# Kernel optimization log

Hardware: AMD Instinct MI355X
Metric: run time of the kernel (lower is better)

Reference implementation:

```python
import jax, jax.numpy as jnp
import numpy as np

B, L, D, NLAYERS, KCONV = 8, 2048, 1024, 3, 4


def setup_inputs() -> dict:
    key = jax.random.key(0)
    ks = jax.random.split(key, 8)
    inp = {
        "x": jax.random.normal(ks[0], (B, L, D), jnp.float32),
        "conv_w": jax.random.normal(ks[1], (NLAYERS, D, KCONV), jnp.float32) * 0.02,
        "conv_b": jnp.zeros((NLAYERS, D), jnp.float32),
        "wr_w": jax.random.normal(ks[2], (NLAYERS, D, D), jnp.float32) * (1.0 / np.sqrt(D)),
        "wr_b": jnp.zeros((NLAYERS, D), jnp.float32),
        "wi_w": jax.random.normal(ks[3], (NLAYERS, D, D), jnp.float32) * (1.0 / np.sqrt(D)),
        "wi_b": jnp.zeros((NLAYERS, D), jnp.float32),
        "log_a": 3.0 + 0.1 * jax.random.normal(ks[4], (NLAYERS, D), jnp.float32),
        "wo_w": jax.random.normal(ks[5], (NLAYERS, D, D), jnp.float32) * (1.0 / np.sqrt(D)),
        "norm_w": jnp.ones((NLAYERS, D), jnp.float32),
        "norm_out_w": jnp.ones((D,), jnp.float32),
    }
    return inp


def _rmsnorm(x, w, eps=1e-6):
    return x * w * jax.lax.rsqrt(jnp.mean(x * x, axis=-1, keepdims=True) + eps)


def _parallel_scan(a, b):
    # h_t = a_t * h_{t-1} + b_t  via log-space prefix scan (h0 = 0)
    a32 = a.astype(jnp.float32)
    b32 = b.astype(jnp.float32)
    log_A = jnp.cumsum(jnp.log(jnp.maximum(a32, 1e-7)), axis=1)
    log_A = jnp.maximum(log_A, -80.0)  # a<=1 so log_A<=0 already
    A = jnp.exp(log_A)
    h = A * jnp.cumsum(b32 * jnp.exp(-log_A), axis=1)
    return h.astype(a.dtype)


def _rglru_layer(x, cw, cb, wrw, wrb, wiw, wib, la, wow, nw):
    # causal depthwise conv1d, kernel 4, left pad 3
    Lx = x.shape[1]
    xp = jnp.pad(x, ((0, 0), (KCONV - 1, 0), (0, 0)))
    x_conv = cb + sum(xp[:, k:k + Lx, :] * cw[:, k] for k in range(KCONV))
    r_t = jax.nn.sigmoid(x_conv @ wrw.T + wrb)
    i_t = jax.nn.sigmoid(x_conv @ wiw.T + wib)
    a_base = jax.nn.sigmoid(la.astype(jnp.float32)).astype(x.dtype)
    a_t = a_base ** (8.0 * r_t)
    b_t = jnp.sqrt(jnp.clip(1.0 - a_t * a_t, 1e-6, None)) * (i_t * x_conv)
    h = _parallel_scan(a_t, b_t)
    return _rmsnorm(h @ wow.T, nw)


def reference(x, conv_w, conv_b, wr_w, wr_b, wi_w, wi_b, log_a, wo_w, norm_w, norm_out_w):
    h = x
    for l in range(NLAYERS):
        h = _rglru_layer(h, conv_w[l], conv_b[l], wr_w[l], wr_b[l],
                         wi_w[l], wi_b[l], log_a[l], wo_w[l], norm_w[l])
    return _rmsnorm(h, norm_out_w)
```

## Files before the change

### kernel.cpp

```cpp
#include <hip/hip_runtime.h>
#include <type_traits>

#define BDIM 8
#define LDIM 2048
#define DDIM 1024
#define NL 3
#define K4 4
#define MDIM (BDIM * LDIM)
#define BK32 32
#define NT32 (DDIM / BK32)

typedef __bf16 bf16x8 __attribute__((ext_vector_type(8)));
typedef __bf16 bf16x4 __attribute__((ext_vector_type(4)));
typedef float f32x4 __attribute__((ext_vector_type(4)));
typedef const __attribute__((address_space(1))) void gvoid_t;
typedef __attribute__((address_space(3))) void svoid_t;

__device__ __forceinline__ void load16(const void* g, void* lds_uniform) {
    __builtin_amdgcn_global_load_lds((gvoid_t*)g, (svoid_t*)lds_uniform, 16, 0, 0);
}

#define SBAR()                                  \
    do {                                        \
        asm volatile("" ::: "memory");          \
        __builtin_amdgcn_s_barrier();           \
        asm volatile("" ::: "memory");          \
    } while (0)
#define WAITV(N) asm volatile("s_waitcnt vmcnt(" #N ")" ::: "memory")
#define LGKM0() asm volatile("s_waitcnt lgkmcnt(0)" ::: "memory")

__global__ void cvt_bf16(const float* __restrict__ s, __bf16* __restrict__ d, int n) {
    int i = blockIdx.x * 256 + threadIdx.x;
    if (i < n) d[i] = (__bf16)s[i];
}

__global__ __launch_bounds__(256) void cvt_interleave(const float* __restrict__ wr,
                                                      const float* __restrict__ wi,
                                                      __bf16* __restrict__ w2, int n) {
    int i = blockIdx.x * 256 + threadIdx.x;
    if (i >= n) return;
    int k = i & (DDIM - 1);
    int ld = i >> 10;
    int l = ld >> 10;
    int d = ld & (DDIM - 1);
    size_t base = ((size_t)l * 2 * DDIM + 2 * d) * DDIM + k;
    w2[base] = (__bf16)wr[i];
    w2[base + DDIM] = (__bf16)wi[i];
}

template <typename T>
__global__ __launch_bounds__(256) void conv_kernel(const T* __restrict__ X,
                                                   const float* __restrict__ cw,
                                                   const float* __restrict__ cb,
                                                   __bf16* __restrict__ XC) {
    int idx = blockIdx.x * 256 + threadIdx.x;
    int d = (idx & (DDIM / 4 - 1)) << 2;
    int t = (idx >> 8) & (LDIM - 1);
    int b = idx >> 19;
    float wv[4][4];
    *(float4*)wv[0] = ((const float4*)cw)[d + 0];
    *(float4*)wv[1] = ((const float4*)cw)[d + 1];
    *(float4*)wv[2] = ((const float4*)cw)[d + 2];
    *(float4*)wv[3] = ((const float4*)cw)[d + 3];
    float4 cbv = *(const float4*)(cb + d);
    float acc[4] = {cbv.x, cbv.y, cbv.z, cbv.w};
#pragma unroll
    for (int k = 0; k < K4; k++) {
        int tt = t + k - (K4 - 1);
        if (tt >= 0) {
            size_t off = ((size_t)(b * LDIM + tt) << 10) + d;
            float xv[4];
            if constexpr (std::is_same<T, float>::value) {
                float4 v = *(const float4*)(X + off);
                xv[0] = v.x; xv[1] = v.y; xv[2] = v.z; xv[3] = v.w;
            } else {
                bf16x4 v = *(const bf16x4*)(X + off);
                xv[0] = (float)v.x; xv[1] = (float)v.y; xv[2] = (float)v.z; xv[3] = (float)v.w;
            }
#pragma unroll
            for (int j = 0; j < 4; j++) acc[j] += xv[j] * wv[j][k];
        }
    }
    bf16x4 o;
    o.x = (__bf16)acc[0]; o.y = (__bf16)acc[1]; o.z = (__bf16)acc[2]; o.w = (__bf16)acc[3];
    *(bf16x4*)(XC + ((size_t)(b * LDIM + t) << 10) + d) = o;
}

__global__ __launch_bounds__(512, 2) void gate_gemm(
    const __bf16* __restrict__ A, const __bf16* __restrict__ W2,
    const float* __restrict__ wrb, const float* __restrict__ wib,
    const float* __restrict__ la,
    __bf16* __restrict__ LOGA, __bf16* __restrict__ BB) {
    __shared__ __attribute__((aligned(16))) __bf16 sm[65536];
    int tid = threadIdx.x;
    int wave = tid >> 6, lane = tid & 63;
    int wm = wave >> 2, wn = wave & 3;
    int fr = lane & 15, quad = lane >> 4;

    int nx = gridDim.x;
    int bid = blockIdx.y * nx + blockIdx.x;
    int cpx = (nx * gridDim.y) >> 3;
    int sw = (bid & 7) * cpx + (bid >> 3);
    int bm0 = (sw / nx) * 256;
    int bn0 = (sw % nx) * 256;

    const __bf16* Ag = A + (size_t)bm0 * DDIM;
    const __bf16* Bg = W2 + (size_t)bn0 * DDIM;

    f32x4 acc[8][4];
    f32x4 zero = {0.f, 0.f, 0.f, 0.f};
#pragma unroll
    for (int i = 0; i < 8; i++)
#pragma unroll
        for (int j = 0; j < 4; j++) acc[i][j] = zero;

    int offA[2][4], offB[4];
#pragma unroll
    for (int mh = 0; mh < 2; mh++)
#pragma unroll
        for (int mi = 0; mi < 4; mi++) {
            int row = wm * 128 + (mh * 4 + mi) * 16 + fr;
            offA[mh][mi] = row * 32 + ((quad ^ ((row >> 1) & 3)) << 3);
        }
#pragma unroll
    for (int ni = 0; ni < 4; ni++) {
        int row = wn * 64 + ni * 16 + fr;
        offB[ni] = 8192 + row * 32 + ((quad ^ ((row >> 1) & 3)) << 3);
    }
    int r0 = tid >> 2, g0 = (tid & 3) ^ ((r0 >> 1) & 3);
    int r1 = (512 + tid) >> 2, g1 = ((512 + tid) & 3) ^ ((r1 >> 1) & 3);
    const __bf16* gA0 = Ag + (size_t)r0 * DDIM + g0 * 8;
    const __bf16* gA1 = Ag + (size_t)r1 * DDIM + g1 * 8;
    const __bf16* gB0 = Bg + (size_t)r0 * DDIM + g0 * 8;
    const __bf16* gB1 = Bg + (size_t)r1 * DDIM + g1 * 8;
    int lb0 = wave * 512, lb1 = 4096 + wave * 512;

    auto STAGEH = [&](int buf, int t, int j) {
        int lo = buf * 16384;
        if (j == 0) {
            load16(gA0 + t * BK32, sm + lo + lb0);
            load16(gB0 + t * BK32, sm + lo + 8192 + lb0);
        } else {
            load16(gA1 + t * BK32, sm + lo + lb1);
            load16(gB1 + t * BK32, sm + lo + 8192 + lb1);
        }
    };
    auto STAGE = [&](int buf, int t) { STAGEH(buf, t, 0); STAGEH(buf, t, 1); };

    STAGE(0, 0);
    STAGE(1, 1);
    STAGE(2, 2);
    for (int t4 = 0; t4 < NT32; t4 += 4) {
#pragma unroll
        for (int tt = 0; tt < 4; tt++) {
            int t = t4 + tt;
            if (t + 2 < NT32) { WAITV(8); }
            else if (t + 1 < NT32) { WAITV(4); }
            else { WAITV(0); }
            SBAR();
            const __bf16* base = sm + tt * 16384;
            int sb = (tt + 3) & 3;
            bf16x8 bfm[4], af[4];
            if (t + 3 < NT32) STAGEH(sb, t + 3, 0);
#pragma unroll
            for (int ni = 0; ni < 4; ni++) bfm[ni] = *(const bf16x8*)(base + offB[ni]);
#pragma unroll
            for (int mi = 0; mi < 4; mi++) af[mi] = *(const bf16x8*)(base + offA[0][mi]);
            SBAR();
            LGKM0();
            __builtin_amdgcn_s_setprio(1);
#pragma unroll
            for (int ni = 0; ni < 4; ni++)
#pragma unroll
                for (int mi = 0; mi < 4; mi++)
                    acc[mi][ni] = __builtin_amdgcn_mfma_f32_16x16x32_bf16(
                        af[mi], bfm[ni], acc[mi][ni], 0, 0, 0);
            __builtin_amdgcn_s_setprio(0);
            SBAR();
            if (t + 3 < NT32) STAGEH(sb, t + 3, 1);
#pragma unroll
            for (int mi = 0; mi < 4; mi++) af[mi] = *(const bf16x8*)(base + offA[1][mi]);
            SBAR();
            LGKM0();
            __builtin_amdgcn_s_setprio(1);
#pragma unroll
            for (int ni = 0; ni < 4; ni++)
#pragma unroll
                for (int mi = 0; mi < 4; mi++)
                    acc[4 + mi][ni] = __builtin_amdgcn_mfma_f32_16x16x32_bf16(
                        af[mi], bfm[ni], acc[4 + mi][ni], 0, 0, 0);
            __builtin_amdgcn_s_setprio(0);
        }
    }

    float* Lt = (float*)&sm[0];
    int colg = (tid & 31) * 8;
    int d0 = (bn0 >> 1) + (colg >> 1);
    float rb[4], ibv[4], lnab[4];
    {
        float4 r4 = *(const float4*)(wrb + d0);
        float4 i4 = *(const float4*)(wib + d0);
        float4 l4 = *(const float4*)(la + d0);
        float lav[4] = {l4.x, l4.y, l4.z, l4.w};
        rb[0] = r4.x; rb[1] = r4.y; rb[2] = r4.z; rb[3] = r4.w;
        ibv[0] = i4.x; ibv[1] = i4.y; ibv[2] = i4.z; ibv[3] = i4.w;
#pragma unroll
        for (int j = 0; j < 4; j++) lnab[j] = __logf(1.f / (1.f + __expf(-lav[j])));
    }
#pragma unroll
    for (int mi = 0; mi < 8; mi++) {
        __syncthreads();
#pragma unroll
        for (int ni = 0; ni < 4; ni++) {
            int col = wn * 64 + ni * 16 + fr;
#pragma unroll
            for (int reg = 0; reg < 4; reg++)
                Lt[(wm * 16 + quad * 4 + reg) * 260 + col] = acc[mi][ni][reg];
        }
        __syncthreads();
#pragma unroll
        for (int hf = 0; hf < 2; hf++) {
            int r = (tid >> 5) + hf * 16;
            int m = bm0 + (r >> 4) * 128 + mi * 16 + (r & 15);
            float vv[8];
            *(f32x4*)&vv[0] = *(const f32x4*)&Lt[r * 260 + colg];
            *(f32x4*)&vv[4] = *(const f32x4*)&Lt[r * 260 + colg + 4];
            bf16x4 xcv = *(const bf16x4*)(A + (size_t)m * DDIM + d0);
            bf16x4 og, ob;
#pragma unroll
            for (int j = 0; j < 4; j++) {
                float rv = 1.f / (1.f + __expf(-(vv[2 * j] + rb[j])));
                float iv = 1.f / (1.f + __expf(-(vv[2 * j + 1] + ibv[j])));
                float lga = 8.f * rv * lnab[j];
                float a = __expf(lga);
                float bt = sqrtf(fmaxf(1.f - a * a, 1e-6f)) * (iv * (float)xcv[j]);
                og[j] = (__bf16)lga;
                ob[j] = (__bf16)bt;
            }
            *(bf16x4*)(LOGA + (size_t)m * DDIM + d0) = og;
            *(bf16x4*)(BB + (size_t)m * DDIM + d0) = ob;
        }
    }
}

__global__ __launch_bounds__(512, 2) void out_gemm(
    const __bf16* __restrict__ A, const __bf16* __restrict__ Wo, __bf16* __restrict__ HW) {
    __shared__ __attribute__((aligned(16))) __bf16 sm[65536];
    int tid = threadIdx.x;
    int wave = tid >> 6, lane = tid & 63;
    int wm = wave >> 2, wn = wave & 3;
    int fr = lane & 15, quad = lane >> 4;

    int nx = gridDim.x;
    int bid = blockIdx.y * nx + blockIdx.x;
    int cpx = (nx * gridDim.y) >> 3;
    int sw = (bid & 7) * cpx + (bid >> 3);
    int bm0 = (sw / nx) * 256;
    int bn0 = (sw % nx) * 256;

    const __bf16* Ag = A + (size_t)bm0 * DDIM;
    const __bf16* Bg = Wo + (size_t)bn0 * DDIM;

    f32x4 acc[8][4];
    f32x4 zero = {0.f, 0.f, 0.f, 0.f};
#pragma unroll
    for (int i = 0; i < 8; i++)
#pragma unroll
        for (int j = 0; j < 4; j++) acc[i][j] = zero;

    int offA[2][4], offB[4];
#pragma unroll
    for (int mh = 0; mh < 2; mh++)
#pragma unroll
        for (int mi = 0; mi < 4; mi++) {
            int row = wm * 128 + (mh * 4 + mi) * 16 + fr;
            offA[mh][mi] = row * 32 + ((quad ^ ((row >> 1) & 3)) << 3);
        }
#pragma unroll
    for (int ni = 0; ni < 4; ni++) {
        int row = wn * 64 + ni * 16 + fr;
        offB[ni] = 8192 + row * 32 + ((quad ^ ((row >> 1) & 3)) << 3);
    }
    int r0 = tid >> 2, g0 = (tid & 3) ^ ((r0 >> 1) & 3);
    int r1 = (512 + tid) >> 2, g1 = ((512 + tid) & 3) ^ ((r1 >> 1) & 3);
    const __bf16* gA0 = Ag + (size_t)r0 * DDIM + g0 * 8;
    const __bf16* gA1 = Ag + (size_t)r1 * DDIM + g1 * 8;
    const __bf16* gB0 = Bg + (size_t)r0 * DDIM + g0 * 8;
    const __bf16* gB1 = Bg + (size_t)r1 * DDIM + g1 * 8;
    int lb0 = wave * 512, lb1 = 4096 + wave * 512;

    auto STAGEH = [&](int buf, int t, int j) {
        int lo = buf * 16384;
        if (j == 0) {
            load16(gA0 + t * BK32, sm + lo + lb0);
            load16(gB0 + t * BK32, sm + lo + 8192 + lb0);
        } else {
            load16(gA1 + t * BK32, sm + lo + lb1);
            load16(gB1 + t * BK32, sm + lo + 8192 + lb1);
        }
    };
    auto STAGE = [&](int buf, int t) { STAGEH(buf, t, 0); STAGEH(buf, t, 1); };

    STAGE(0, 0);
    STAGE(1, 1);
    STAGE(2, 2);
    for (int t4 = 0; t4 < NT32; t4 += 4) {
#pragma unroll
        for (int tt = 0; tt < 4; tt++) {
            int t = t4 + tt;
            if (t + 2 < NT32) { WAITV(8); }
            else if (t + 1 < NT32) { WAITV(4); }
            else { WAITV(0); }
            SBAR();
            const __bf16* base = sm + tt * 16384;
            int sb = (tt + 3) & 3;
            bf16x8 bfm[4], af[4];
            if (t + 3 < NT32) STAGEH(sb, t + 3, 0);
#pragma unroll
            for (int ni = 0; ni < 4; ni++) bfm[ni] = *(const bf16x8*)(base + offB[ni]);
#pragma unroll
            for (int mi = 0; mi < 4; mi++) af[mi] = *(const bf16x8*)(base + offA[0][mi]);
            SBAR();
            LGKM0();
            __builtin_amdgcn_s_setprio(1);
#pragma unroll
            for (int ni = 0; ni < 4; ni++)
#pragma unroll
                for (int mi = 0; mi < 4; mi++)
                    acc[mi][ni] = __builtin_amdgcn_mfma_f32_16x16x32_bf16(
                        af[mi], bfm[ni], acc[mi][ni], 0, 0, 0);
            __builtin_amdgcn_s_setprio(0);
            SBAR();
            if (t + 3 < NT32) STAGEH(sb, t + 3, 1);
#pragma unroll
            for (int mi = 0; mi < 4; mi++) af[mi] = *(const bf16x8*)(base + offA[1][mi]);
            SBAR();
            LGKM0();
            __builtin_amdgcn_s_setprio(1);
#pragma unroll
            for (int ni = 0; ni < 4; ni++)
#pragma unroll
                for (int mi = 0; mi < 4; mi++)
                    acc[4 + mi][ni] = __builtin_amdgcn_mfma_f32_16x16x32_bf16(
                        af[mi], bfm[ni], acc[4 + mi][ni], 0, 0, 0);
            __builtin_amdgcn_s_setprio(0);
        }
    }

    float* Lt = (float*)&sm[0];
    int colg = (tid & 31) * 8;
    int n0 = bn0 + colg;
#pragma unroll
    for (int mi = 0; mi < 8; mi++) {
        __syncthreads();
#pragma unroll
        for (int ni = 0; ni < 4; ni++) {
            int col = wn * 64 + ni * 16 + fr;
#pragma unroll
            for (int reg = 0; reg < 4; reg++)
                Lt[(wm * 16 + quad * 4 + reg) * 260 + col] = acc[mi][ni][reg];
        }
        __syncthreads();
#pragma unroll
        for (int hf = 0; hf < 2; hf++) {
            int r = (tid >> 5) + hf * 16;
            int m = bm0 + (r >> 4) * 128 + mi * 16 + (r & 15);
            float vv[8];
            *(f32x4*)&vv[0] = *(const f32x4*)&Lt[r * 260 + colg];
            *(f32x4*)&vv[4] = *(const f32x4*)&Lt[r * 260 + colg + 4];
            bf16x8 o;
#pragma unroll
            for (int j = 0; j < 8; j++) o[j] = (__bf16)vv[j];
            *(bf16x8*)(HW + (size_t)m * DDIM + n0) = o;
        }
    }
}

#define SCH 32
#define SCT 64
__global__ __launch_bounds__(1024) void scan_kernel(const __bf16* __restrict__ LOGA,
                                                    const __bf16* __restrict__ BB,
                                                    __bf16* __restrict__ H) {
    int b = blockIdx.y;
    int dl = threadIdx.x & 31;
    int d = blockIdx.x * 32 + dl;
    int c = threadIdx.x >> 5;
    size_t base = ((size_t)b * LDIM + (size_t)c * SCT) * DDIM + d;
    const __bf16* pga = LOGA + base;
    const __bf16* pbb = BB + base;
    __bf16* pH = H + base;

    float S = 0.f;
#pragma unroll 8
    for (int t = 0; t < SCT; t++) S += (float)pga[(size_t)t * DDIM];
    __shared__ float sS[SCH][32];
    sS[c][dl] = S;
    __syncthreads();
    float L0 = 0.f;
    for (int cc = 0; cc < c; cc++) L0 += sS[cc][dl];

    float Lr = L0, lcp = fmaxf(L0, -80.f), hB = 0.f;
#pragma unroll 4
    for (int t = 0; t < SCT; t++) {
        float lga = (float)pga[(size_t)t * DDIM];
        Lr += lga;
        float lc = fmaxf(Lr, -80.f);
        hB = __expf(lc - lcp) * hB + (float)pbb[(size_t)t * DDIM];
        lcp = lc;
    }
    float Ac = __expf(fmaxf(Lr, -80.f) - fmaxf(L0, -80.f));
    __shared__ float sA[SCH][32], sB[SCH][32];
    sA[c][dl] = Ac;
    sB[c][dl] = hB;
    __syncthreads();
    float hin = 0.f;
    for (int cc = 0; cc < c; cc++) hin = sA[cc][dl] * hin + sB[cc][dl];

    Lr = L0;
    lcp = fmaxf(L0, -80.f);
    float h = hin;
#pragma unroll 4
    for (int t = 0; t < SCT; t++) {
        float lga = (float)pga[(size_t)t * DDIM];
        Lr += lga;
        float lc = fmaxf(Lr, -80.f);
        h = __expf(lc - lcp) * h + (float)pbb[(size_t)t * DDIM];
        lcp = lc;
        pH[(size_t)t * DDIM] = (__bf16)h;
    }
}

template <typename TI, typename TO>
__global__ __launch_bounds__(256) void rmsnorm_kernel(const TI* __restrict__ X,
                                                      const float* __restrict__ w,
                                                      TO* __restrict__ Y) {
    int row = blockIdx.x;
    int tid = threadIdx.x;
    size_t off = (size_t)row * DDIM + tid * 4;
    float v[4];
    if constexpr (std::is_same<TI, float>::value) {
        float4 t = *(const float4*)(X + off);
        v[0] = t.x; v[1] = t.y; v[2] = t.z; v[3] = t.w;
    } else {
        bf16x4 t = *(const bf16x4*)(X + off);
        v[0] = (float)t.x; v[1] = (float)t.y; v[2] = (float)t.z; v[3] = (float)t.w;
    }
    float s = v[0] * v[0] + v[1] * v[1] + v[2] * v[2] + v[3] * v[3];
#pragma unroll
    for (int o = 32; o > 0; o >>= 1) s += __shfl_down(s, o);
    __shared__ float sw[4];
    if ((tid & 63) == 0) sw[tid >> 6] = s;
    __syncthreads();
    float tot = sw[0] + sw[1] + sw[2] + sw[3];
    float scale = rsqrtf(tot * (1.f / (float)DDIM) + 1e-6f);
    float4 wv = ((const float4*)w)[tid];
    float o0 = v[0] * wv.x * scale, o1 = v[1] * wv.y * scale;
    float o2 = v[2] * wv.z * scale, o3 = v[3] * wv.w * scale;
    if constexpr (std::is_same<TO, float>::value) {
        float4 o = {o0, o1, o2, o3};
        *(float4*)(Y + off) = o;
    } else {
        bf16x4 o;
        o.x = (__bf16)o0; o.y = (__bf16)o1; o.z = (__bf16)o2; o.w = (__bf16)o3;
        *(bf16x4*)(Y + off) = o;
    }
}

extern "C" void kernel_launch(void* const* d_in, const int* in_sizes, int n_in,
                              void* d_out, int out_size, void* d_ws, size_t ws_size,
                              hipStream_t stream) {
    const float* x = (const float*)d_in[0];
    const float* conv_w = (const float*)d_in[1];
    const float* conv_b = (const float*)d_in[2];
    const float* wr_w = (const float*)d_in[3];
    const float* wr_b = (const float*)d_in[4];
    const float* wi_w = (const float*)d_in[5];
    const float* wi_b = (const float*)d_in[6];
    const float* log_a = (const float*)d_in[7];
    const float* wo_w = (const float*)d_in[8];
    const float* norm_w = (const float*)d_in[9];
    const float* norm_out_w = (const float*)d_in[10];

    const size_t W2SZ = (size_t)NL * 2 * DDIM * DDIM;
    const size_t WOSZ = (size_t)NL * DDIM * DDIM;
    const size_t MD = (size_t)MDIM * DDIM;
    __bf16* w2 = (__bf16*)d_ws;
    __bf16* wo16 = w2 + W2SZ;
    __bf16* XC = wo16 + WOSZ;
    __bf16* LGA = XC + MD;
    __bf16* BBf = LGA + MD;
    __bf16* Hb = BBf + MD;
    __bf16* HWb = Hb + MD;
    __bf16* PNb = HWb + MD;

    int nw = (int)WOSZ;
    cvt_interleave<<<(nw + 255) / 256, 256, 0, stream>>>(wr_w, wi_w, w2, nw);
    cvt_bf16<<<(nw + 255) / 256, 256, 0, stream>>>(wo_w, wo16, nw);

    for (int l = 0; l < NL; l++) {
        if (l == 0)
            conv_kernel<float><<<(MDIM * (DDIM / 4)) / 256, 256, 0, stream>>>(
                x, conv_w, conv_b, XC);
        else
            conv_kernel<__bf16><<<(MDIM * (DDIM / 4)) / 256, 256, 0, stream>>>(
                PNb, conv_w + (size_t)l * DDIM * K4, conv_b + (size_t)l * DDIM, XC);
        gate_gemm<<<dim3(2 * DDIM / 256, MDIM / 256), 512, 0, stream>>>(
            XC, w2 + (size_t)l * 2 * DDIM * DDIM,
            wr_b + (size_t)l * DDIM, wi_b + (size_t)l * DDIM, log_a + (size_t)l * DDIM,
            LGA, BBf);
        scan_kernel<<<dim3(DDIM / 32, BDIM), 1024, 0, stream>>>(LGA, BBf, Hb);
        out_gemm<<<dim3(DDIM / 256, MDIM / 256), 512, 0, stream>>>(
            Hb, wo16 + (size_t)l * DDIM * DDIM, HWb);
        rmsnorm_kernel<__bf16, __bf16><<<MDIM, 256, 0, stream>>>(
            HWb, norm_w + (size_t)l * DDIM, PNb);
    }
    rmsnorm_kernel<__bf16, float><<<MDIM, 256, 0, stream>>>(PNb, norm_out_w, (float*)d_out);
}
```

Measured before the change: 919.0 us.

## Cut per-tile barriers to one and issue LDS reads via inline asm

Both GEMM main loops now use a single workgroup barrier per K-tile instead of four. All four global-to-LDS prefetch loads for tile t+3 are issued together right after that barrier. LDS fragment reads go through inline ds_read_b128 with precomputed LDS byte addresses, and sched_barrier fences keep the compiler from reordering them around the MFMA blocks. This removes barrier stalls and the split-stage ping-pong in exchange for less forced wave interleaving. Correctness relies on the 4-buffer ring and the vmcnt waits to keep buffers from being overwritten while other waves still read them.

```diff
diff --git a/kernel.cpp b/kernel.cpp
--- a/kernel.cpp
+++ b/kernel.cpp
@@ -28,6 +28,16 @@
     } while (0)
 #define WAITV(N) asm volatile("s_waitcnt vmcnt(" #N ")" ::: "memory")
 #define LGKM0() asm volatile("s_waitcnt lgkmcnt(0)" ::: "memory")
+#define SCHED0() __builtin_amdgcn_sched_barrier(0)
+
+__device__ __forceinline__ unsigned lds_addr(const void* p) {
+    return (unsigned)(unsigned long long)(svoid_t*)(p);
+}
+__device__ __forceinline__ bf16x8 dsr16(unsigned a) {
+    f32x4 r;
+    asm volatile("ds_read_b128 %0, %1" : "=v"(r) : "v"(a));
+    return __builtin_bit_cast(bf16x8, r);
+}
 
 __global__ void cvt_bf16(const float* __restrict__ s, __bf16* __restrict__ d, int n) {
     int i = blockIdx.x * 256 + threadIdx.x;
@@ -114,18 +124,19 @@
 #pragma unroll
         for (int j = 0; j < 4; j++) acc[i][j] = zero;
 
-    int offA[2][4], offB[4];
+    unsigned smb = lds_addr(sm);
+    unsigned adA[2][4], adB[4];
 #pragma unroll
     for (int mh = 0; mh < 2; mh++)
 #pragma unroll
         for (int mi = 0; mi < 4; mi++) {
             int row = wm * 128 + (mh * 4 + mi) * 16 + fr;
-            offA[mh][mi] = row * 32 + ((quad ^ ((row >> 1) & 3)) << 3);
+            adA[mh][mi] = smb + 2u * (row * 32 + ((quad ^ ((row >> 1) & 3)) << 3));
         }
 #pragma unroll
     for (int ni = 0; ni < 4; ni++) {
         int row = wn * 64 + ni * 16 + fr;
-        offB[ni] = 8192 + row * 32 + ((quad ^ ((row >> 1) & 3)) << 3);
+        adB[ni] = smb + 2u * (8192 + row * 32 + ((quad ^ ((row >> 1) & 3)) << 3));
     }
     int r0 = tid >> 2, g0 = (tid & 3) ^ ((r0 >> 1) & 3);
     int r1 = (512 + tid) >> 2, g1 = ((512 + tid) & 3) ^ ((r1 >> 1) & 3);
@@ -135,17 +146,13 @@
     const __bf16* gB1 = Bg + (size_t)r1 * DDIM + g1 * 8;
     int lb0 = wave * 512, lb1 = 4096 + wave * 512;
 
-    auto STAGEH = [&](int buf, int t, int j) {
+    auto STAGE = [&](int buf, int t) {
         int lo = buf * 16384;
-        if (j == 0) {
-            load16(gA0 + t * BK32, sm + lo + lb0);
-            load16(gB0 + t * BK32, sm + lo + 8192 + lb0);
-        } else {
-            load16(gA1 + t * BK32, sm + lo + lb1);
-            load16(gB1 + t * BK32, sm + lo + 8192 + lb1);
-        }
+        load16(gA0 + t * BK32, sm + lo + lb0);
+        load16(gA1 + t * BK32, sm + lo + lb1);
+        load16(gB0 + t * BK32, sm + lo + 8192 + lb0);
+        load16(gB1 + t * BK32, sm + lo + 8192 + lb1);
     };
-    auto STAGE = [&](int buf, int t) { STAGEH(buf, t, 0); STAGEH(buf, t, 1); };
 
     STAGE(0, 0);
     STAGE(1, 1);
@@ -158,16 +165,15 @@
             else if (t + 1 < NT32) { WAITV(4); }
             else { WAITV(0); }
             SBAR();
-            const __bf16* base = sm + tt * 16384;
-            int sb = (tt + 3) & 3;
+            if (t + 3 < NT32) STAGE((tt + 3) & 3, t + 3);
+            unsigned tb = (unsigned)(tt * 32768);
             bf16x8 bfm[4], af[4];
-            if (t + 3 < NT32) STAGEH(sb, t + 3, 0);
-#pragma unroll
-            for (int ni = 0; ni < 4; ni++) bfm[ni] = *(const bf16x8*)(base + offB[ni]);
-#pragma unroll
-            for (int mi = 0; mi < 4; mi++) af[mi] = *(const bf16x8*)(base + offA[0][mi]);
-            SBAR();
+#pragma unroll
+            for (int ni = 0; ni < 4; ni++) bfm[ni] = dsr16(adB[ni] + tb);
+#pragma unroll
+            for (int mi = 0; mi < 4; mi++) af[mi] = dsr16(adA[0][mi] + tb);
             LGKM0();
+            SCHED0();
             __builtin_amdgcn_s_setprio(1);
 #pragma unroll
             for (int ni = 0; ni < 4; ni++)
@@ -176,12 +182,10 @@
                     acc[mi][ni] = __builtin_amdgcn_mfma_f32_16x16x32_bf16(
                         af[mi], bfm[ni], acc[mi][ni], 0, 0, 0);
             __builtin_amdgcn_s_setprio(0);
-            SBAR();
-            if (t + 3 < NT32) STAGEH(sb, t + 3, 1);
-#pragma unroll
-            for (int mi = 0; mi < 4; mi++) af[mi] = *(const bf16x8*)(base + offA[1][mi]);
-            SBAR();
+#pragma unroll
+            for (int mi = 0; mi < 4; mi++) af[mi] = dsr16(adA[1][mi] + tb);
             LGKM0();
+            SCHED0();
             __builtin_amdgcn_s_setprio(1);
 #pragma unroll
             for (int ni = 0; ni < 4; ni++)
@@ -268,18 +272,19 @@
 #pragma unroll
         for (int j = 0; j < 4; j++) acc[i][j] = zero;
 
-    int offA[2][4], offB[4];
+    unsigned smb = lds_addr(sm);
+    unsigned adA[2][4], adB[4];
 #pragma unroll
     for (int mh = 0; mh < 2; mh++)
 #pragma unroll
         for (int mi = 0; mi < 4; mi++) {
             int row = wm * 128 + (mh * 4 + mi) * 16 + fr;
-            offA[mh][mi] = row * 32 + ((quad ^ ((row >> 1) & 3)) << 3);
+            adA[mh][mi] = smb + 2u * (row * 32 + ((quad ^ ((row >> 1) & 3)) << 3));
         }
 #pragma unroll
     for (int ni = 0; ni < 4; ni++) {
         int row = wn * 64 + ni * 16 + fr;
-        offB[ni] = 8192 + row * 32 + ((quad ^ ((row >> 1) & 3)) << 3);
+        adB[ni] = smb + 2u * (8192 + row * 32 + ((quad ^ ((row >> 1) & 3)) << 3));
     }
     int r0 = tid >> 2, g0 = (tid & 3) ^ ((r0 >> 1) & 3);
     int r1 = (512 + tid) >> 2, g1 = ((512 + tid) & 3) ^ ((r1 >> 1) & 3);
@@ -289,17 +294,13 @@
     const __bf16* gB1 = Bg + (size_t)r1 * DDIM + g1 * 8;
     int lb0 = wave * 512, lb1 = 4096 + wave * 512;
 
-    auto STAGEH = [&](int buf, int t, int j) {
+    auto STAGE = [&](int buf, int t) {
         int lo = buf * 16384;
-        if (j == 0) {
-            load16(gA0 + t * BK32, sm + lo + lb0);
-            load16(gB0 + t * BK32, sm + lo + 8192 + lb0);
-        } else {
-            load16(gA1 + t * BK32, sm + lo + lb1);
-            load16(gB1 + t * BK32, sm + lo + 8192 + lb1);
-        }
+        load16(gA0 + t * BK32, sm + lo + lb0);
+        load16(gA1 + t * BK32, sm + lo + lb1);
+        load16(gB0 + t * BK32, sm + lo + 8192 + lb0);
+        load16(gB1 + t * BK32, sm + lo + 8192 + lb1);
     };
-    auto STAGE = [&](int buf, int t) { STAGEH(buf, t, 0); STAGEH(buf, t, 1); };
 
     STAGE(0, 0);
     STAGE(1, 1);
@@ -312,16 +313,15 @@
             else if (t + 1 < NT32) { WAITV(4); }
             else { WAITV(0); }
             SBAR();
-            const __bf16* base = sm + tt * 16384;
-            int sb = (tt + 3) & 3;
+            if (t + 3 < NT32) STAGE((tt + 3) & 3, t + 3);
+            unsigned tb = (unsigned)(tt * 32768);
             bf16x8 bfm[4], af[4];
-            if (t + 3 < NT32) STAGEH(sb, t + 3, 0);
-#pragma unroll
-            for (int ni = 0; ni < 4; ni++) bfm[ni] = *(const bf16x8*)(base + offB[ni]);
-#pragma unroll
-            for (int mi = 0; mi < 4; mi++) af[mi] = *(const bf16x8*)(base + offA[0][mi]);
-            SBAR();
+#pragma unroll
+            for (int ni = 0; ni < 4; ni++) bfm[ni] = dsr16(adB[ni] + tb);
+#pragma unroll
+            for (int mi = 0; mi < 4; mi++) af[mi] = dsr16(adA[0][mi] + tb);
             LGKM0();
+            SCHED0();
             __builtin_amdgcn_s_setprio(1);
 #pragma unroll
             for (int ni = 0; ni < 4; ni++)
@@ -330,12 +330,10 @@
                     acc[mi][ni] = __builtin_amdgcn_mfma_f32_16x16x32_bf16(
                         af[mi], bfm[ni], acc[mi][ni], 0, 0, 0);
             __builtin_amdgcn_s_setprio(0);
-            SBAR();
-            if (t + 3 < NT32) STAGEH(sb, t + 3, 1);
-#pragma unroll
-            for (int mi = 0; mi < 4; mi++) af[mi] = *(const bf16x8*)(base + offA[1][mi]);
-            SBAR();
+#pragma unroll
+            for (int mi = 0; mi < 4; mi++) af[mi] = dsr16(adA[1][mi] + tb);
             LGKM0();
+            SCHED0();
             __builtin_amdgcn_s_setprio(1);
 #pragma unroll
             for (int ni = 0; ni < 4; ni++)
```

Result: no change. 912.1 us (-0.8%).
